# Optimization experiments

Measured on AMD Instinct MI355X. Metric: run time of the kernel, lower is better.

## Reference

```python
import jax, jax.numpy as jnp
import numpy as np

N_NODES = 100000
N_EDGES = 1600000
IN_CH = 128
OUT_CH = 32
HEADS = 4
NEG_SLOPE = 0.2


def setup_inputs() -> dict:
    key = jax.random.key(0)
    k1, k2, k3, k4 = jax.random.split(key, 4)
    x = jax.random.normal(k1, (N_NODES, IN_CH), dtype=jnp.float32)
    # xavier-ish scale for params
    weight = jax.random.normal(k2, (IN_CH, HEADS * OUT_CH), dtype=jnp.float32) * 0.1
    att = jax.random.normal(k3, (1, HEADS, 2 * OUT_CH), dtype=jnp.float32) * 0.1
    edge_index = jax.random.randint(k4, (2, N_EDGES), 0, N_NODES, dtype=jnp.int64)
    return {"x": x, "weight": weight, "att": att, "edge_index": edge_index}


def reference(x, weight, att, edge_index):
    num_nodes = x.shape[0]
    # project and split heads: [N, H, C]
    h = jnp.matmul(x, weight).reshape(num_nodes, HEADS, OUT_CH)
    row, col = edge_index[0], edge_index[1]
    x_i = h[row]   # [E, H, C]
    x_j = h[col]   # [E, H, C]
    # alpha_e = sum_c att[:, :, :C]*x_i + att[:, :, C:]*x_j  -> [E, H]
    a_i = att[0, :, :OUT_CH]   # [H, C]
    a_j = att[0, :, OUT_CH:]   # [H, C]
    alpha = jnp.einsum('ehc,hc->eh', x_i, a_i) + jnp.einsum('ehc,hc->eh', x_j, a_j)
    alpha = jnp.where(alpha >= 0, alpha, NEG_SLOPE * alpha)  # leaky_relu
    # segment softmax over destination node (col)
    amax = jax.ops.segment_max(alpha, col, num_segments=num_nodes)  # [N, H]
    amax = jnp.where(jnp.isfinite(amax), amax, 0.0)  # empty segments -> 0
    e = jnp.exp(alpha - amax[col])
    s = jax.ops.segment_sum(e, col, num_segments=num_nodes)  # [N, H]
    alpha = e / (s[col] + 1e-16)
    # weighted aggregation: scatter-add x_j * alpha to destination nodes
    msg = x_j * alpha[:, :, None]  # [E, H, C]
    out = jax.ops.segment_sum(msg, col, num_segments=num_nodes)  # [N, H, C]
    # concat=True
    return out.reshape(num_nodes, HEADS * OUT_CH)
```

## Files before the change

### kernel.cpp

```cpp
#include <hip/hip_runtime.h>
#include <hip/hip_bf16.h>

#define N_NODES 100000
#define N_EDGES 1600000
#define K_DIM 128
#define N_DIM 128
#define BM_WORDS 3125
#define PART_STRIDE 3136
#define FLAG_BLOCKS 256
#define PART_OFF 4096
#define BROWS 128
#define LDA 136

typedef __attribute__((ext_vector_type(8))) short bf16x8;
typedef __attribute__((ext_vector_type(4))) float f32x4;

__device__ inline unsigned short f2bf(float f) {
    __hip_bfloat16 b = __float2bfloat16(f);
    return __builtin_bit_cast(unsigned short, b);
}

__global__ __launch_bounds__(256)
void flag_partial(const int* __restrict__ ei, unsigned int* __restrict__ parts) {
    __shared__ unsigned int lbm[BM_WORDS];
    for (int i = threadIdx.x; i < BM_WORDS; i += 256) lbm[i] = 0;
    __syncthreads();

    bool is64 = ((ei[1] | ei[3] | ei[5] | ei[7]) == 0);
    const int base = blockIdx.x * (N_EDGES / FLAG_BLOCKS);
    if (is64) {
        const uint4* p = (const uint4*)(ei + 2 * N_EDGES + 2 * base);
        for (int t = threadIdx.x; t < 3125; t += 256) {
            uint4 v = p[t];
            atomicOr(&lbm[v.x >> 5], 1u << (v.x & 31));
            atomicOr(&lbm[v.z >> 5], 1u << (v.z & 31));
        }
    } else {
        const uint2* p = (const uint2*)(ei + N_EDGES + base);
        for (int t = threadIdx.x; t < 3125; t += 256) {
            uint2 v = p[t];
            atomicOr(&lbm[v.x >> 5], 1u << (v.x & 31));
            atomicOr(&lbm[v.y >> 5], 1u << (v.y & 31));
        }
    }
    __syncthreads();

    unsigned int* dst = parts + (size_t)blockIdx.x * PART_STRIDE;
    for (int i = threadIdx.x; i < BM_WORDS; i += 256) dst[i] = lbm[i];
}

__global__ __launch_bounds__(256, 2)
void gemm_fused(const float* __restrict__ xf,
                const float* __restrict__ wf,
                const unsigned int* __restrict__ parts,
                float* __restrict__ out) {
    __shared__ __attribute__((aligned(16))) unsigned short ldsW[N_DIM * LDA];
    __shared__ __attribute__((aligned(16))) unsigned short ldsA[BROWS * LDA];
    __shared__ unsigned int lmask[4][4];

    const int tid  = threadIdx.x;
    const int lane = tid & 63;
    const int wave = tid >> 6;
    const int rb0  = blockIdx.x * BROWS;

    {
        const unsigned int* p =
            parts + (size_t)tid * PART_STRIDE + blockIdx.x * 4;
        uint4 pv = *(const uint4*)p;
#pragma unroll
        for (int off = 32; off; off >>= 1) {
            pv.x |= __shfl_xor(pv.x, off);
            pv.y |= __shfl_xor(pv.y, off);
            pv.z |= __shfl_xor(pv.z, off);
            pv.w |= __shfl_xor(pv.w, off);
        }
        if (lane == 0) {
            lmask[wave][0] = pv.x; lmask[wave][1] = pv.y;
            lmask[wave][2] = pv.z; lmask[wave][3] = pv.w;
        }
    }

#pragma unroll
    for (int i = 0; i < 8; ++i) {
        int c  = i * 256 + tid;
        int n  = c & 127;
        int k0 = (c >> 7) << 3;
        unsigned short tmp[8];
#pragma unroll
        for (int j = 0; j < 8; ++j) tmp[j] = f2bf(wf[(k0 + j) * N_DIM + n]);
        *(uint4*)(ldsW + n * LDA + k0) = *(const uint4*)tmp;
    }

#pragma unroll
    for (int i = 0; i < 16; ++i) {
        int f  = i * 256 + tid;
        int rl = f >> 5;
        int c4 = f & 31;
        int rg = rb0 + rl;
        if (rg >= N_NODES) rg = N_NODES - 1;
        f32x4 v = *(const f32x4*)(xf + (size_t)rg * K_DIM + c4 * 4);
        unsigned short t4[4];
#pragma unroll
        for (int j = 0; j < 4; ++j) t4[j] = f2bf(v[j]);
        *(uint2*)(ldsA + rl * LDA + c4 * 4) = *(const uint2*)t4;
    }
    __syncthreads();

    const int m    = lane & 15;
    const int quad = lane >> 4;
    const int rowb = wave * 32;

    f32x4 acc[2][8];
#pragma unroll
    for (int mt = 0; mt < 2; ++mt)
#pragma unroll
        for (int t = 0; t < 8; ++t) acc[mt][t] = (f32x4){0.f, 0.f, 0.f, 0.f};

#pragma unroll
    for (int kk = 0; kk < 4; ++kk) {
        const int kbase = kk * 32 + quad * 8;
        bf16x8 af[2];
#pragma unroll
        for (int mt = 0; mt < 2; ++mt)
            af[mt] = *(const bf16x8*)(ldsA + (rowb + mt * 16 + m) * LDA + kbase);
#pragma unroll
        for (int t = 0; t < 8; ++t) {
            bf16x8 bfrag = *(const bf16x8*)(ldsW + (t * 16 + m) * LDA + kbase);
#pragma unroll
            for (int mt = 0; mt < 2; ++mt)
                acc[mt][t] = __builtin_amdgcn_mfma_f32_16x16x32_bf16(
                    af[mt], bfrag, acc[mt][t], 0, 0, 0);
        }
    }

    const unsigned int fm = lmask[0][wave] | lmask[1][wave] |
                            lmask[2][wave] | lmask[3][wave];

#pragma unroll
    for (int mt = 0; mt < 2; ++mt) {
#pragma unroll
        for (int r = 0; r < 4; ++r) {
            int lrow = rowb + mt * 16 + quad * 4 + r;
            int orow = rb0 + lrow;
            if (orow < N_NODES) {
                float fmul = ((fm >> (lrow & 31)) & 1) ? 1.0f : 0.0f;
#pragma unroll
                for (int t = 0; t < 8; ++t)
                    out[(size_t)orow * N_DIM + t * 16 + m] = acc[mt][t][r] * fmul;
            }
        }
    }
}

extern "C" void kernel_launch(void* const* d_in, const int* in_sizes, int n_in,
                              void* d_out, int out_size, void* d_ws, size_t ws_size,
                              hipStream_t stream) {
    const float* x = (const float*)d_in[0];
    const float* w = (const float*)d_in[1];
    const int* ei = (const int*)d_in[3];
    float* out = (float*)d_out;

    unsigned int* parts = (unsigned int*)d_ws + PART_OFF;

    flag_partial<<<FLAG_BLOCKS, 256, 0, stream>>>(ei, parts);
    gemm_fused<<<(N_NODES + BROWS - 1) / BROWS, 256, 0, stream>>>(x, w, parts, out);
}
```

Baseline: 121.6 us.

## Halve GEMM row tile and replace LDS padding with XOR swizzle

Shrinks the per-block row tile from 128 to 64, so each wave computes one 16-row MFMA tile instead of two. The launch bound rises from 2 to 3 blocks per SIMD group, and the grid doubles. The padded LDS layout is replaced by an XOR-swizzled unpadded layout, which saves shared memory and avoids bank conflicts. The goal is higher occupancy and better latency hiding in this memory-bound projection, at the cost of each block reconverting the full weight matrix twice as often overall.

```diff
diff --git a/kernel.cpp b/kernel.cpp
--- a/kernel.cpp
+++ b/kernel.cpp
@@ -9,8 +9,7 @@
 #define PART_STRIDE 3136
 #define FLAG_BLOCKS 256
 #define PART_OFF 4096
-#define BROWS 128
-#define LDA 136
+#define BROWS 64
 
 typedef __attribute__((ext_vector_type(8))) short bf16x8;
 typedef __attribute__((ext_vector_type(4))) float f32x4;
@@ -49,14 +48,14 @@
     for (int i = threadIdx.x; i < BM_WORDS; i += 256) dst[i] = lbm[i];
 }
 
-__global__ __launch_bounds__(256, 2)
+__global__ __launch_bounds__(256, 3)
 void gemm_fused(const float* __restrict__ xf,
                 const float* __restrict__ wf,
                 const unsigned int* __restrict__ parts,
                 float* __restrict__ out) {
-    __shared__ __attribute__((aligned(16))) unsigned short ldsW[N_DIM * LDA];
-    __shared__ __attribute__((aligned(16))) unsigned short ldsA[BROWS * LDA];
-    __shared__ unsigned int lmask[4][4];
+    __shared__ __attribute__((aligned(16))) unsigned short ldsW[N_DIM * 128];
+    __shared__ __attribute__((aligned(16))) unsigned short ldsA[BROWS * 128];
+    __shared__ unsigned int lmask[4][2];
 
     const int tid  = threadIdx.x;
     const int lane = tid & 63;
@@ -65,19 +64,14 @@
 
     {
         const unsigned int* p =
-            parts + (size_t)tid * PART_STRIDE + blockIdx.x * 4;
-        uint4 pv = *(const uint4*)p;
+            parts + (size_t)tid * PART_STRIDE + blockIdx.x * 2;
+        uint2 pv = *(const uint2*)p;
 #pragma unroll
         for (int off = 32; off; off >>= 1) {
             pv.x |= __shfl_xor(pv.x, off);
             pv.y |= __shfl_xor(pv.y, off);
-            pv.z |= __shfl_xor(pv.z, off);
-            pv.w |= __shfl_xor(pv.w, off);
         }
-        if (lane == 0) {
-            lmask[wave][0] = pv.x; lmask[wave][1] = pv.y;
-            lmask[wave][2] = pv.z; lmask[wave][3] = pv.w;
-        }
+        if (lane == 0) { lmask[wave][0] = pv.x; lmask[wave][1] = pv.y; }
     }
 
 #pragma unroll
@@ -88,66 +82,69 @@
         unsigned short tmp[8];
 #pragma unroll
         for (int j = 0; j < 8; ++j) tmp[j] = f2bf(wf[(k0 + j) * N_DIM + n]);
-        *(uint4*)(ldsW + n * LDA + k0) = *(const uint4*)tmp;
+        int byte = n * 256 + k0 * 2;
+        byte ^= (n & 7) << 4;
+        *(uint4*)((char*)ldsW + byte) = *(const uint4*)tmp;
     }
 
 #pragma unroll
-    for (int i = 0; i < 16; ++i) {
-        int f  = i * 256 + tid;
-        int rl = f >> 5;
-        int c4 = f & 31;
+    for (int i = 0; i < 4; ++i) {
+        int c  = i * 256 + tid;
+        int rl = c >> 4;
+        int k8 = c & 15;
         int rg = rb0 + rl;
         if (rg >= N_NODES) rg = N_NODES - 1;
-        f32x4 v = *(const f32x4*)(xf + (size_t)rg * K_DIM + c4 * 4);
-        unsigned short t4[4];
+        f32x4 v0 = *(const f32x4*)(xf + (size_t)rg * K_DIM + k8 * 8);
+        f32x4 v1 = *(const f32x4*)(xf + (size_t)rg * K_DIM + k8 * 8 + 4);
+        unsigned short t8[8];
 #pragma unroll
-        for (int j = 0; j < 4; ++j) t4[j] = f2bf(v[j]);
-        *(uint2*)(ldsA + rl * LDA + c4 * 4) = *(const uint2*)t4;
+        for (int j = 0; j < 4; ++j) {
+            t8[j]     = f2bf(v0[j]);
+            t8[4 + j] = f2bf(v1[j]);
+        }
+        int byte = rl * 256 + k8 * 16;
+        byte ^= (rl & 7) << 4;
+        *(uint4*)((char*)ldsA + byte) = *(const uint4*)t8;
     }
     __syncthreads();
 
     const int m    = lane & 15;
     const int quad = lane >> 4;
-    const int rowb = wave * 32;
+    const int arow = wave * 16 + m;
 
-    f32x4 acc[2][8];
+    f32x4 acc[8];
 #pragma unroll
-    for (int mt = 0; mt < 2; ++mt)
-#pragma unroll
-        for (int t = 0; t < 8; ++t) acc[mt][t] = (f32x4){0.f, 0.f, 0.f, 0.f};
+    for (int t = 0; t < 8; ++t) acc[t] = (f32x4){0.f, 0.f, 0.f, 0.f};
 
 #pragma unroll
     for (int kk = 0; kk < 4; ++kk) {
         const int kbase = kk * 32 + quad * 8;
-        bf16x8 af[2];
-#pragma unroll
-        for (int mt = 0; mt < 2; ++mt)
-            af[mt] = *(const bf16x8*)(ldsA + (rowb + mt * 16 + m) * LDA + kbase);
+        int abyte = (arow * 128 + kbase) * 2;
+        abyte ^= (arow & 7) << 4;
+        bf16x8 af = *(const bf16x8*)((const char*)ldsA + abyte);
 #pragma unroll
         for (int t = 0; t < 8; ++t) {
-            bf16x8 bfrag = *(const bf16x8*)(ldsW + (t * 16 + m) * LDA + kbase);
-#pragma unroll
-            for (int mt = 0; mt < 2; ++mt)
-                acc[mt][t] = __builtin_amdgcn_mfma_f32_16x16x32_bf16(
-                    af[mt], bfrag, acc[mt][t], 0, 0, 0);
+            int bn = t * 16 + m;
+            int bbyte = (bn * 128 + kbase) * 2;
+            bbyte ^= (bn & 7) << 4;
+            bf16x8 bfrag = *(const bf16x8*)((const char*)ldsW + bbyte);
+            acc[t] = __builtin_amdgcn_mfma_f32_16x16x32_bf16(af, bfrag, acc[t], 0, 0, 0);
         }
     }
 
-    const unsigned int fm = lmask[0][wave] | lmask[1][wave] |
-                            lmask[2][wave] | lmask[3][wave];
+    const unsigned int fm0 = lmask[0][0] | lmask[1][0] | lmask[2][0] | lmask[3][0];
+    const unsigned int fm1 = lmask[0][1] | lmask[1][1] | lmask[2][1] | lmask[3][1];
 
 #pragma unroll
-    for (int mt = 0; mt < 2; ++mt) {
+    for (int r = 0; r < 4; ++r) {
+        int lrow = wave * 16 + quad * 4 + r;
+        int orow = rb0 + lrow;
+        if (orow < N_NODES) {
+            unsigned int w = (lrow & 32) ? fm1 : fm0;
+            float fmul = ((w >> (lrow & 31)) & 1) ? 1.0f : 0.0f;
 #pragma unroll
-        for (int r = 0; r < 4; ++r) {
-            int lrow = rowb + mt * 16 + quad * 4 + r;
-            int orow = rb0 + lrow;
-            if (orow < N_NODES) {
-                float fmul = ((fm >> (lrow & 31)) & 1) ? 1.0f : 0.0f;
-#pragma unroll
-                for (int t = 0; t < 8; ++t)
-                    out[(size_t)orow * N_DIM + t * 16 + m] = acc[mt][t][r] * fmul;
-            }
+            for (int t = 0; t < 8; ++t)
+                out[(size_t)orow * N_DIM + t * 16 + m] = acc[t][r] * fmul;
         }
     }
 }
```

Result: no change. 121.6 us (+0.0%).
